# Kernel tuning notes

Measured on AMD Instinct MI355X. Metric: run time of the kernel, lower is better.

## Reference

```python
import jax, jax.numpy as jnp
import numpy as np
from jax import lax

NEG = -1.0e9


def setup_inputs() -> dict:
    key = jax.random.key(0)
    ks = jax.random.split(key, 12)
    B, S, d, H = 4, 1024, 1024, 16
    sc = 1.0 / np.sqrt(d)
    inp = {
        "query": jax.random.normal(ks[0], (B, S, d), jnp.float32),
        "key": jax.random.normal(ks[1], (B, S, d), jnp.float32),
        "value": jax.random.normal(ks[2], (B, S, d), jnp.float32),
        # causal mask: True = masked (future positions)
        "mask": jnp.triu(jnp.ones((S, S), bool), k=1)[None, None],
        "Wq": jax.random.normal(ks[3], (d, d), jnp.float32) * sc,
        "bq": jnp.zeros((d,), jnp.float32),
        "Wk": jax.random.normal(ks[4], (d, d), jnp.float32) * sc,
        "bk": jnp.zeros((d,), jnp.float32),
        "Wv": jax.random.normal(ks[5], (d, d), jnp.float32) * sc,
        "bv": jnp.zeros((d,), jnp.float32),
        "Wo": jax.random.normal(ks[6], (d, d), jnp.float32) * sc,
        "bo": jnp.zeros((d,), jnp.float32),
        "gammas": jax.random.uniform(ks[7], (H, 1, 1), jnp.float32, -0.05, 0.05),
    }
    return inp


def reference(query, key, value, mask, Wq, bq, Wk, bk, Wv, bv, Wo, bo, gammas):
    B, S, d = query.shape
    H = gammas.shape[0]
    dk = d // H

    def proj(x, W, b):
        # [B,S,d] -> [B,H,S,dk]
        return (x @ W.T + b).reshape(B, S, H, dk).transpose(0, 2, 1, 3)

    q = proj(query, Wq, bq)
    k = proj(key, Wk, bk)
    v = proj(value, Wv, bv)

    scores = jnp.einsum("bhqd,bhkd->bhqk", q, k) / np.float32(np.sqrt(dk))

    # --- distance-decay effect (no-grad block in torch) ---
    p = jax.nn.softmax(jnp.where(mask, NEG, scores), axis=-1)
    distcum = jnp.cumsum(p, axis=-1)
    disttot = jnp.sum(p, axis=-1, keepdims=True)
    idx = jnp.arange(S, dtype=scores.dtype)
    pos = jnp.abs(idx[:, None] - idx[None, :])[None, None]  # [1,1,S,S]
    dist = jnp.sqrt(jnp.clip((disttot - distcum) * pos, 0.0))
    dist = lax.stop_gradient(dist)

    gamma = -jnp.abs(gammas)[None]  # [1,H,1,1]
    total_effect = jnp.clip(jnp.exp(dist * gamma), 1e-5, 1e5)

    gated = jnp.where(mask, NEG, scores * total_effect)
    attn = jax.nn.softmax(gated, axis=-1)
    attn = jnp.where(mask, 0.0, attn)

    out = jnp.einsum("bhqk,bhkd->bhqd", attn, v)
    out = out.transpose(0, 2, 1, 3).reshape(B, S, d)
    out = out @ Wo.T + bo
    return out, attn
```

## Files before the change

kernel.cpp:

```cpp
#include <hip/hip_runtime.h>
#include <hip/hip_bf16.h>

typedef __attribute__((ext_vector_type(8))) short short8;
typedef __attribute__((ext_vector_type(4))) float f32x4;
typedef __attribute__((ext_vector_type(4))) unsigned short us4;

#define MFMA(a, b, c) __builtin_amdgcn_mfma_f32_16x16x32_bf16((a), (b), (c), 0, 0, 0)

static __device__ inline unsigned short f2b(float f) {
    __hip_bfloat16 h = __float2bfloat16(f);
    return *reinterpret_cast<unsigned short*>(&h);
}
static __device__ inline float b2f(unsigned short u) {
    unsigned int x = ((unsigned int)u) << 16;
    return __builtin_bit_cast(float, x);
}

static __device__ __forceinline__ void gload_lds16(const unsigned short* g, unsigned short* s) {
    __builtin_amdgcn_global_load_lds(
        (const __attribute__((address_space(1))) unsigned int*)(g),
        (__attribute__((address_space(3))) unsigned int*)(s),
        16, 0, 0);
}

__global__ __launch_bounds__(256) void convk(
    const float* __restrict__ a, const float* __restrict__ b,
    const float* __restrict__ c, const float* __restrict__ dd,
    unsigned short* oa, unsigned short* ob, unsigned short* oc, unsigned short* od, int n)
{
    const float* in; unsigned short* out;
    switch (blockIdx.y) {
        case 0: in = a; out = oa; break;
        case 1: in = b; out = ob; break;
        case 2: in = c; out = oc; break;
        default: in = dd; out = od; break;
    }
    int i = (blockIdx.x * 256 + threadIdx.x) * 4;
    if (i >= n) return;
    float4 v = *(const float4*)(in + i);
    us4 o;
    o[0] = f2b(v.x); o[1] = f2b(v.y); o[2] = f2b(v.z); o[3] = f2b(v.w);
    *(us4*)(out + i) = o;
}

template<int EMODE>
__global__ __launch_bounds__(256) void gemm_bt(
    const unsigned short* __restrict__ A,
    const unsigned short* __restrict__ Bm,
    const float* __restrict__ bias,
    float* __restrict__ Cf,
    unsigned short* __restrict__ Cb,
    int M, int N, int K)
{
    __shared__ unsigned short sA[2][64 * 32];
    __shared__ unsigned short sB[2][128 * 32];
    const int tid = threadIdx.x;
    const int wave = tid >> 6, lane = tid & 63;
    const int wm = (wave >> 1) * 32, wn = (wave & 1) * 64;
    const int bm = blockIdx.x * 64, bn = blockIdx.y * 128;
    const int fr = lane & 15, fg = lane >> 4;

    const int srow = lane >> 2, schk = (lane & 3) * 8;
    const unsigned short* Ab  = A  + (size_t)(bm + wave * 16 + srow) * K + schk;
    const unsigned short* Bb0 = Bm + (size_t)(bn + wave * 32 + srow) * K + schk;
    const unsigned short* Bb1 = Bb0 + (size_t)16 * K;
    const int aw = (wave * 16) * 32, bw0 = (wave * 32) * 32, bw1 = (wave * 32 + 16) * 32;

    f32x4 acc[2][4] = {};
    const int nt = K >> 5;

    gload_lds16(Ab, &sA[0][aw]);
    gload_lds16(Bb0, &sB[0][bw0]);
    gload_lds16(Bb1, &sB[0][bw1]);
    __syncthreads();

    int cur = 0;
    for (int t = 0; t < nt; ++t) {
        if (t + 1 < nt) {
            int kt = (t + 1) << 5;
            gload_lds16(Ab + kt, &sA[cur ^ 1][aw]);
            gload_lds16(Bb0 + kt, &sB[cur ^ 1][bw0]);
            gload_lds16(Bb1 + kt, &sB[cur ^ 1][bw1]);
        }
        short8 af[2], bf[4];
        #pragma unroll
        for (int mr = 0; mr < 2; ++mr) af[mr] = *(const short8*)&sA[cur][(wm + mr * 16 + fr) * 32 + fg * 8];
        #pragma unroll
        for (int nr = 0; nr < 4; ++nr) bf[nr] = *(const short8*)&sB[cur][(wn + nr * 16 + fr) * 32 + fg * 8];
        #pragma unroll
        for (int mr = 0; mr < 2; ++mr)
            #pragma unroll
            for (int nr = 0; nr < 4; ++nr)
                acc[mr][nr] = MFMA(af[mr], bf[nr], acc[mr][nr]);
        __syncthreads();
        cur ^= 1;
    }

    #pragma unroll
    for (int mr = 0; mr < 2; ++mr)
        #pragma unroll
        for (int nr = 0; nr < 4; ++nr)
            #pragma unroll
            for (int j = 0; j < 4; ++j) {
                int m = bm + wm + mr * 16 + fg * 4 + j;
                int n = bn + wn + nr * 16 + fr;
                float v = acc[mr][nr][j] + bias[n];
                if (EMODE == 0) {
                    Cf[(size_t)m * N + n] = v;
                } else if (EMODE == 1) {
                    int b = m >> 10, s = m & 1023, h = n >> 6, dc = n & 63;
                    Cb[(((size_t)(b * 16 + h)) * 1024 + s) * 64 + dc] = f2b(v);
                } else {
                    int b = m >> 10, s = m & 1023, h = n >> 6, dc = n & 63;
                    Cb[(((size_t)(b * 16 + h)) * 64 + dc) * 1024 + s] = f2b(v);
                }
            }
}

__global__ __launch_bounds__(256) void attn_fused(
    const unsigned short* __restrict__ Qh,
    const unsigned short* __restrict__ Kh,
    const unsigned short* __restrict__ Vt,
    const float* __restrict__ gammas,
    float* __restrict__ attn_out,
    unsigned short* __restrict__ ctx)
{
    extern __shared__ char smem[];
    const int RS = 1032;
    unsigned short* s_s = (unsigned short*)smem;
    unsigned short* s_q = (unsigned short*)(smem + 16 * RS * 2);
    float* s_inv = (float*)(smem + 16 * RS * 2 + 16 * 72 * 2);
    const int S = 1024;

    int gid = blockIdx.y * gridDim.x + blockIdx.x;
    int jj = gid >> 3;
    const int bh = (gid & 7) * 8 + (jj >> 6);
    const int qb = jj & 63;
    const int q0 = qb * 16;
    const int tid = threadIdx.x;
    const int wave = tid >> 6, lane = tid & 63, fr = lane & 15, fg = lane >> 4;

    {
        int rr = tid >> 4, c4 = (tid & 15) * 4;
        *(uint2*)&s_q[rr * 72 + c4] = *(const uint2*)&Qh[((size_t)bh * S + q0 + rr) * 64 + c4];
    }
    __syncthreads();
    const int kmax = q0 + 15;

    {
        short8 qf0 = *(const short8*)&s_q[fr * 72 + fg * 8];
        short8 qf1 = *(const short8*)&s_q[fr * 72 + 32 + fg * 8];
        const unsigned short* kbase = &Kh[(size_t)bh * S * 64];
        for (int nf = 0; nf < 16; ++nf) {
            int cb = (nf * 4 + wave) * 16;
            if (cb > kmax) break;
            const unsigned short* kb = kbase + (size_t)cb * 64;
            short8 kf0 = *(const short8*)&kb[fr * 64 + fg * 8];
            short8 kf1 = *(const short8*)&kb[fr * 64 + 32 + fg * 8];
            f32x4 a = {0.f, 0.f, 0.f, 0.f};
            a = MFMA(qf0, kf0, a);
            a = MFMA(qf1, kf1, a);
            #pragma unroll
            for (int j = 0; j < 4; ++j)
                s_s[(size_t)(fg * 4 + j) * RS + cb + fr] = f2b(a[j] * 0.125f);
        }
    }
    __syncthreads();

    {
        const int r = tid >> 4, sub = tid & 15;
        const int qr = q0 + r;
        unsigned short* srow = &s_s[(size_t)r * RS];
        const float ag = fabsf(gammas[bh & 15]);
        const int m = ((qb + 4) >> 2) | 1;
        const int L = 4 * m;
        const int base = sub * L;

        float seg = 0.f;
        for (int c = 0; c < m; ++c) {
            us4 s4 = *(const us4*)&srow[base + c * 4];
            #pragma unroll
            for (int j = 0; j < 4; ++j) {
                int kk = base + c * 4 + j;
                seg += (kk <= qr) ? __expf(b2f(s4[j])) : 0.f;
            }
        }
        float x = seg, t;
        t = __shfl_up(x, 1, 16); if (sub >= 1) x += t;
        t = __shfl_up(x, 2, 16); if (sub >= 2) x += t;
        t = __shfl_up(x, 4, 16); if (sub >= 4) x += t;
        t = __shfl_up(x, 8, 16); if (sub >= 8) x += t;
        const float T = __shfl(x, 15, 16);
        const float invT = 1.f / T;
        float run = x - seg;

        float ls2 = 0.f;
        for (int c = 0; c < m; ++c) {
            us4 s4 = *(const us4*)&srow[base + c * 4];
            us4 o;
            #pragma unroll
            for (int j = 0; j < 4; ++j) {
                int kk = base + c * 4 + j;
                bool act = kk <= qr;
                float s = b2f(s4[j]);
                float e = act ? __expf(s) : 0.f;
                run += e;
                float rem = fmaxf(T - run, 0.f) * invT;
                float dist = sqrtf(rem * (float)(qr - kk));
                float te = __expf(-ag * dist);
                float e2 = act ? __expf(s * te) : 0.f;
                o[j] = f2b(e2);
                ls2 += e2;
            }
            *(us4*)&srow[base + c * 4] = o;
        }
        us4 z = {0, 0, 0, 0};
        for (int c = 4 * L + sub; c < 256; c += 16)
            *(us4*)&srow[c * 4] = z;
        #pragma unroll
        for (int mm = 1; mm < 16; mm <<= 1) ls2 += __shfl_xor(ls2, mm, 16);
        if (sub == 0) s_inv[r] = 1.f / ls2;
    }
    __syncthreads();

    for (int r2 = 0; r2 < 16; ++r2) {
        us4 e4 = *(const us4*)&s_s[(size_t)r2 * RS + tid * 4];
        float iv = s_inv[r2];
        f32x4 w = {b2f(e4[0]) * iv, b2f(e4[1]) * iv, b2f(e4[2]) * iv, b2f(e4[3]) * iv};
        __builtin_nontemporal_store(w,
            (f32x4*)(attn_out + ((size_t)bh * S + q0 + r2) * S + tid * 4));
    }

    {
        const unsigned short* vb = &Vt[(size_t)bh * 64 * S];
        f32x4 acc = {0.f, 0.f, 0.f, 0.f};
        const int ktiles = (kmax + 32) >> 5;
        const unsigned short* prow = &s_s[(size_t)fr * RS];
        for (int kt = 0; kt < ktiles; ++kt) {
            short8 pa = *(const short8*)&prow[kt * 32 + fg * 8];
            short8 vf = *(const short8*)&vb[(size_t)(wave * 16 + fr) * S + kt * 32 + fg * 8];
            acc = MFMA(pa, vf, acc);
        }
        int b = bh >> 4, h = bh & 15;
        #pragma unroll
        for (int j = 0; j < 4; ++j) {
            float iv = s_inv[fg * 4 + j];
            ctx[((size_t)b * S + q0 + fg * 4 + j) * 1024 + h * 64 + wave * 16 + fr] = f2b(acc[j] * iv);
        }
    }
}

extern "C" void kernel_launch(void* const* d_in, const int* in_sizes, int n_in,
                              void* d_out, int out_size, void* d_ws, size_t ws_size,
                              hipStream_t stream) {
    const float* query  = (const float*)d_in[0];
    const float* key    = (const float*)d_in[1];
    const float* value  = (const float*)d_in[2];
    const float* Wq = (const float*)d_in[4];
    const float* bq = (const float*)d_in[5];
    const float* Wk = (const float*)d_in[6];
    const float* bk = (const float*)d_in[7];
    const float* Wv = (const float*)d_in[8];
    const float* bv = (const float*)d_in[9];
    const float* Wo = (const float*)d_in[10];
    const float* bo = (const float*)d_in[11];
    const float* gammas = (const float*)d_in[12];

    const int S = 1024, dmodel = 1024;
    const int M = 4 * S;
    const size_t MD = (size_t)M * dmodel;
    const size_t DD = (size_t)dmodel * dmodel;

    char* ws = (char*)d_ws;
    unsigned short* xq  = (unsigned short*)ws;            ws += MD * 2;
    unsigned short* xk  = (unsigned short*)ws;            ws += MD * 2;
    unsigned short* xv  = (unsigned short*)ws;            ws += MD * 2;
    unsigned short* wqb = (unsigned short*)ws;            ws += DD * 2;
    unsigned short* wkb = (unsigned short*)ws;            ws += DD * 2;
    unsigned short* wvb = (unsigned short*)ws;            ws += DD * 2;
    unsigned short* wob = (unsigned short*)ws;            ws += DD * 2;
    unsigned short* qh  = (unsigned short*)ws;            ws += MD * 2;
    unsigned short* kh  = (unsigned short*)ws;            ws += MD * 2;
    unsigned short* vt  = (unsigned short*)ws;            ws += MD * 2;
    unsigned short* ctx = (unsigned short*)ws;            ws += MD * 2;

    float* outp = (float*)d_out;
    float* attn_out = outp + MD;

    convk<<<dim3(4096, 3), 256, 0, stream>>>(query, key, value, nullptr, xq, xk, xv, nullptr, (int)MD);
    convk<<<dim3(1024, 4), 256, 0, stream>>>(Wq, Wk, Wv, Wo, wqb, wkb, wvb, wob, (int)DD);

    gemm_bt<1><<<dim3(64, 8), 256, 0, stream>>>(xq, wqb, bq, nullptr, qh, M, dmodel, dmodel);
    gemm_bt<1><<<dim3(64, 8), 256, 0, stream>>>(xk, wkb, bk, nullptr, kh, M, dmodel, dmodel);
    gemm_bt<2><<<dim3(64, 8), 256, 0, stream>>>(xv, wvb, bv, nullptr, vt, M, dmodel, dmodel);

    size_t lds = 16 * 1032 * 2 + 16 * 72 * 2 + 16 * 4;
    attn_fused<<<dim3(64, 64), 256, lds, stream>>>(qh, kh, vt, gammas, attn_out, ctx);

    gemm_bt<0><<<dim3(64, 8), 256, 0, stream>>>(ctx, wob, bo, outp, nullptr, M, dmodel, dmodel);
}
```

Measured before the change: 195.0 us.

## Merge conversion and QKV GEMM launches and triple-buffer GEMM loads

Merges the two fp32-to-bf16 conversion launches into one 7-way grid and the three Q/K/V projection GEMMs into one z-indexed launch. This cuts launch overhead and lets more blocks run concurrently. The GEMM main loop moves from double to triple buffering, with a prefetch distance of two tiles, explicit vmcnt waits and raw s_barrier calls in place of __syncthreads. Risks are the extra LDS per block, which may lower occupancy, and whether the hand-written waitcnt counts correctly guard the global-to-LDS loads.

```diff
diff --git a/kernel.cpp b/kernel.cpp
--- a/kernel.cpp
+++ b/kernel.cpp
@@ -24,16 +24,22 @@
 }
 
 __global__ __launch_bounds__(256) void convk(
-    const float* __restrict__ a, const float* __restrict__ b,
-    const float* __restrict__ c, const float* __restrict__ dd,
-    unsigned short* oa, unsigned short* ob, unsigned short* oc, unsigned short* od, int n)
-{
-    const float* in; unsigned short* out;
+    const float* __restrict__ i0, const float* __restrict__ i1, const float* __restrict__ i2,
+    const float* __restrict__ i3, const float* __restrict__ i4, const float* __restrict__ i5,
+    const float* __restrict__ i6,
+    unsigned short* o0, unsigned short* o1, unsigned short* o2, unsigned short* o3,
+    unsigned short* o4, unsigned short* o5, unsigned short* o6,
+    int nbig, int nsmall)
+{
+    const float* in; unsigned short* out; int n;
     switch (blockIdx.y) {
-        case 0: in = a; out = oa; break;
-        case 1: in = b; out = ob; break;
-        case 2: in = c; out = oc; break;
-        default: in = dd; out = od; break;
+        case 0: in = i0; out = o0; n = nbig; break;
+        case 1: in = i1; out = o1; n = nbig; break;
+        case 2: in = i2; out = o2; n = nbig; break;
+        case 3: in = i3; out = o3; n = nsmall; break;
+        case 4: in = i4; out = o4; n = nsmall; break;
+        case 5: in = i5; out = o5; n = nsmall; break;
+        default: in = i6; out = o6; n = nsmall; break;
     }
     int i = (blockIdx.x * 256 + threadIdx.x) * 4;
     if (i >= n) return;
@@ -43,21 +49,19 @@
     *(us4*)(out + i) = o;
 }
 
-template<int EMODE>
-__global__ __launch_bounds__(256) void gemm_bt(
+__device__ __forceinline__ void gemm_body(
     const unsigned short* __restrict__ A,
     const unsigned short* __restrict__ Bm,
     const float* __restrict__ bias,
     float* __restrict__ Cf,
     unsigned short* __restrict__ Cb,
-    int M, int N, int K)
-{
-    __shared__ unsigned short sA[2][64 * 32];
-    __shared__ unsigned short sB[2][128 * 32];
+    int emode, int M, int N, int K, int bmx, int bnx,
+    unsigned short (*sA)[64 * 32], unsigned short (*sB)[128 * 32])
+{
     const int tid = threadIdx.x;
     const int wave = tid >> 6, lane = tid & 63;
     const int wm = (wave >> 1) * 32, wn = (wave & 1) * 64;
-    const int bm = blockIdx.x * 64, bn = blockIdx.y * 128;
+    const int bm = bmx * 64, bn = bnx * 128;
     const int fr = lane & 15, fg = lane >> 4;
 
     const int srow = lane >> 2, schk = (lane & 3) * 8;
@@ -69,19 +73,30 @@
     f32x4 acc[2][4] = {};
     const int nt = K >> 5;
 
-    gload_lds16(Ab, &sA[0][aw]);
-    gload_lds16(Bb0, &sB[0][bw0]);
-    gload_lds16(Bb1, &sB[0][bw1]);
-    __syncthreads();
-
-    int cur = 0;
+    gload_lds16(Ab,       &sA[0][aw]);
+    gload_lds16(Bb0,      &sB[0][bw0]);
+    gload_lds16(Bb1,      &sB[0][bw1]);
+    gload_lds16(Ab + 32,  &sA[1][aw]);
+    gload_lds16(Bb0 + 32, &sB[1][bw0]);
+    gload_lds16(Bb1 + 32, &sB[1][bw1]);
+
     for (int t = 0; t < nt; ++t) {
-        if (t + 1 < nt) {
-            int kt = (t + 1) << 5;
-            gload_lds16(Ab + kt, &sA[cur ^ 1][aw]);
-            gload_lds16(Bb0 + kt, &sB[cur ^ 1][bw0]);
-            gload_lds16(Bb1 + kt, &sB[cur ^ 1][bw1]);
-        }
+        const int cur = t % 3;
+        if (t + 2 < nt) {
+            const int nxt = (t + 2) % 3;
+            const int kt = (t + 2) << 5;
+            gload_lds16(Ab + kt,  &sA[nxt][aw]);
+            gload_lds16(Bb0 + kt, &sB[nxt][bw0]);
+            gload_lds16(Bb1 + kt, &sB[nxt][bw1]);
+            asm volatile("s_waitcnt vmcnt(6)" ::: "memory");
+        } else if (t + 1 < nt) {
+            asm volatile("s_waitcnt vmcnt(3)" ::: "memory");
+        } else {
+            asm volatile("s_waitcnt vmcnt(0)" ::: "memory");
+        }
+        __builtin_amdgcn_s_barrier();
+        __builtin_amdgcn_sched_barrier(0);
+
         short8 af[2], bf[4];
         #pragma unroll
         for (int mr = 0; mr < 2; ++mr) af[mr] = *(const short8*)&sA[cur][(wm + mr * 16 + fr) * 32 + fg * 8];
@@ -92,8 +107,9 @@
             #pragma unroll
             for (int nr = 0; nr < 4; ++nr)
                 acc[mr][nr] = MFMA(af[mr], bf[nr], acc[mr][nr]);
-        __syncthreads();
-        cur ^= 1;
+
+        __builtin_amdgcn_s_barrier();
+        __builtin_amdgcn_sched_barrier(0);
     }
 
     #pragma unroll
@@ -105,9 +121,9 @@
                 int m = bm + wm + mr * 16 + fg * 4 + j;
                 int n = bn + wn + nr * 16 + fr;
                 float v = acc[mr][nr][j] + bias[n];
-                if (EMODE == 0) {
+                if (emode == 0) {
                     Cf[(size_t)m * N + n] = v;
-                } else if (EMODE == 1) {
+                } else if (emode == 1) {
                     int b = m >> 10, s = m & 1023, h = n >> 6, dc = n & 63;
                     Cb[(((size_t)(b * 16 + h)) * 1024 + s) * 64 + dc] = f2b(v);
                 } else {
@@ -115,6 +131,36 @@
                     Cb[(((size_t)(b * 16 + h)) * 64 + dc) * 1024 + s] = f2b(v);
                 }
             }
+}
+
+__global__ __launch_bounds__(256) void gemm_qkv(
+    const unsigned short* __restrict__ xq, const unsigned short* __restrict__ xk,
+    const unsigned short* __restrict__ xv,
+    const unsigned short* __restrict__ wq, const unsigned short* __restrict__ wk,
+    const unsigned short* __restrict__ wv,
+    const float* __restrict__ bq, const float* __restrict__ bk, const float* __restrict__ bv,
+    unsigned short* __restrict__ qh, unsigned short* __restrict__ kh,
+    unsigned short* __restrict__ vt,
+    int M, int N, int K)
+{
+    __shared__ unsigned short sA[3][64 * 32];
+    __shared__ unsigned short sB[3][128 * 32];
+    const int z = blockIdx.z;
+    const unsigned short* A  = z == 0 ? xq : z == 1 ? xk : xv;
+    const unsigned short* Bm = z == 0 ? wq : z == 1 ? wk : wv;
+    const float* bias        = z == 0 ? bq : z == 1 ? bk : bv;
+    unsigned short* Cb       = z == 0 ? qh : z == 1 ? kh : vt;
+    gemm_body(A, Bm, bias, nullptr, Cb, z == 2 ? 2 : 1, M, N, K,
+              blockIdx.x, blockIdx.y, sA, sB);
+}
+
+__global__ __launch_bounds__(256) void gemm_wo(
+    const unsigned short* __restrict__ A, const unsigned short* __restrict__ Bm,
+    const float* __restrict__ bias, float* __restrict__ Cf, int M, int N, int K)
+{
+    __shared__ unsigned short sA[3][64 * 32];
+    __shared__ unsigned short sB[3][128 * 32];
+    gemm_body(A, Bm, bias, Cf, nullptr, 0, M, N, K, blockIdx.x, blockIdx.y, sA, sB);
 }
 
 __global__ __launch_bounds__(256) void attn_fused(
@@ -287,15 +333,15 @@
     float* outp = (float*)d_out;
     float* attn_out = outp + MD;
 
-    convk<<<dim3(4096, 3), 256, 0, stream>>>(query, key, value, nullptr, xq, xk, xv, nullptr, (int)MD);
-    convk<<<dim3(1024, 4), 256, 0, stream>>>(Wq, Wk, Wv, Wo, wqb, wkb, wvb, wob, (int)DD);
-
-    gemm_bt<1><<<dim3(64, 8), 256, 0, stream>>>(xq, wqb, bq, nullptr, qh, M, dmodel, dmodel);
-    gemm_bt<1><<<dim3(64, 8), 256, 0, stream>>>(xk, wkb, bk, nullptr, kh, M, dmodel, dmodel);
-    gemm_bt<2><<<dim3(64, 8), 256, 0, stream>>>(xv, wvb, bv, nullptr, vt, M, dmodel, dmodel);
+    convk<<<dim3(4096, 7), 256, 0, stream>>>(
+        query, key, value, Wq, Wk, Wv, Wo,
+        xq, xk, xv, wqb, wkb, wvb, wob, (int)MD, (int)DD);
+
+    gemm_qkv<<<dim3(64, 8, 3), 256, 0, stream>>>(
+        xq, xk, xv, wqb, wkb, wvb, bq, bk, bv, qh, kh, vt, M, dmodel, dmodel);
 
     size_t lds = 16 * 1032 * 2 + 16 * 72 * 2 + 16 * 4;
     attn_fused<<<dim3(64, 64), 256, lds, stream>>>(qh, kh, vt, gammas, attn_out, ctx);
 
-    gemm_bt<0><<<dim3(64, 8), 256, 0, stream>>>(ctx, wob, bo, outp, nullptr, M, dmodel, dmodel);
-}
+    gemm_wo<<<dim3(64, 8), 256, 0, stream>>>(ctx, wob, bo, outp, M, dmodel, dmodel);
+}
```

Result: faster. 186.1 us (-4.6%).

## Fuse fp32-to-bf16 input conversion into QKV GEMM and triple-buffer GEMM pipelines

Applied to the files above, without the earlier changes.

The separate conversion kernel for query/key/value is removed. The QKV GEMM now loads fp32 activations into registers, converts them to bf16 and writes them to LDS, and all three projections run in one launch over a z-dimension. Both GEMMs now use a K-step of 64 with a 3-stage LDS ring and explicit vmcnt waits and barriers, so loads for tile t+2 overlap compute on tile t. This drops an extra read/write pass over the activations and two kernel launches, at the cost of more LDS per block and hand-tuned waitcnt logic that is fragile.

```diff
diff --git a/kernel.cpp b/kernel.cpp
--- a/kernel.cpp
+++ b/kernel.cpp
@@ -22,18 +22,22 @@
         (__attribute__((address_space(3))) unsigned int*)(s),
         16, 0, 0);
 }
+#define WAITV(N) asm volatile("s_waitcnt vmcnt(" #N ")" ::: "memory")
+#define WAITL    asm volatile("s_waitcnt lgkmcnt(0)" ::: "memory")
+#define SBAR     __builtin_amdgcn_s_barrier()
+#define SCHED0   __builtin_amdgcn_sched_barrier(0)
 
 __global__ __launch_bounds__(256) void convk(
-    const float* __restrict__ a, const float* __restrict__ b,
-    const float* __restrict__ c, const float* __restrict__ dd,
-    unsigned short* oa, unsigned short* ob, unsigned short* oc, unsigned short* od, int n)
+    const float* __restrict__ i0, const float* __restrict__ i1,
+    const float* __restrict__ i2, const float* __restrict__ i3,
+    unsigned short* o0, unsigned short* o1, unsigned short* o2, unsigned short* o3, int n)
 {
     const float* in; unsigned short* out;
     switch (blockIdx.y) {
-        case 0: in = a; out = oa; break;
-        case 1: in = b; out = ob; break;
-        case 2: in = c; out = oc; break;
-        default: in = dd; out = od; break;
+        case 0: in = i0; out = o0; break;
+        case 1: in = i1; out = o1; break;
+        case 2: in = i2; out = o2; break;
+        default: in = i3; out = o3; break;
     }
     int i = (blockIdx.x * 256 + threadIdx.x) * 4;
     if (i >= n) return;
@@ -43,57 +47,98 @@
     *(us4*)(out + i) = o;
 }
 
-template<int EMODE>
-__global__ __launch_bounds__(256) void gemm_bt(
-    const unsigned short* __restrict__ A,
-    const unsigned short* __restrict__ Bm,
-    const float* __restrict__ bias,
-    float* __restrict__ Cf,
-    unsigned short* __restrict__ Cb,
+__global__ __launch_bounds__(256) void gemm_qkv(
+    const float* __restrict__ Aq, const float* __restrict__ Ak, const float* __restrict__ Av,
+    const unsigned short* __restrict__ wq, const unsigned short* __restrict__ wk,
+    const unsigned short* __restrict__ wv,
+    const float* __restrict__ bq, const float* __restrict__ bk, const float* __restrict__ bv,
+    unsigned short* __restrict__ qh, unsigned short* __restrict__ kh,
+    unsigned short* __restrict__ vt,
     int M, int N, int K)
 {
-    __shared__ unsigned short sA[2][64 * 32];
-    __shared__ unsigned short sB[2][128 * 32];
+    __shared__ unsigned short sA[3][2 * 64 * 32];
+    __shared__ unsigned short sB[3][2 * 128 * 32];
+    const int z = blockIdx.z;
+    const float* A           = z == 0 ? Aq : z == 1 ? Ak : Av;
+    const unsigned short* Bm = z == 0 ? wq : z == 1 ? wk : wv;
+    const float* bias        = z == 0 ? bq : z == 1 ? bk : bv;
+    unsigned short* Cb       = z == 0 ? qh : z == 1 ? kh : vt;
+    const int emode          = z == 2 ? 2 : 1;
+
     const int tid = threadIdx.x;
     const int wave = tid >> 6, lane = tid & 63;
     const int wm = (wave >> 1) * 32, wn = (wave & 1) * 64;
     const int bm = blockIdx.x * 64, bn = blockIdx.y * 128;
     const int fr = lane & 15, fg = lane >> 4;
 
-    const int srow = lane >> 2, schk = (lane & 3) * 8;
-    const unsigned short* Ab  = A  + (size_t)(bm + wave * 16 + srow) * K + schk;
-    const unsigned short* Bb0 = Bm + (size_t)(bn + wave * 32 + srow) * K + schk;
-    const unsigned short* Bb1 = Bb0 + (size_t)16 * K;
-    const int aw = (wave * 16) * 32, bw0 = (wave * 32) * 32, bw1 = (wave * 32 + 16) * 32;
+    const int ar = tid >> 2, ac = (tid & 3) * 16;
+    const float* Ag = A + (size_t)(bm + ar) * K + ac;
+    const int aks = ac >> 5, acol = ac & 31;
+    const int brow = lane >> 2, bchk = (lane & 3) * 8;
+    const unsigned short* Bg = Bm + (size_t)(bn + wave * 32 + brow) * K + bchk;
 
     f32x4 acc[2][4] = {};
-    const int nt = K >> 5;
-
-    gload_lds16(Ab, &sA[0][aw]);
-    gload_lds16(Bb0, &sB[0][bw0]);
-    gload_lds16(Bb1, &sB[0][bw1]);
-    __syncthreads();
-
-    int cur = 0;
+    const int nt = K >> 6;
+
+    float4 rA[4];
+    #define LOAD_A(t)  { const float* p = Ag + ((t) << 6); \
+        rA[0] = *(const float4*)(p); rA[1] = *(const float4*)(p + 4); \
+        rA[2] = *(const float4*)(p + 8); rA[3] = *(const float4*)(p + 12); }
+    #define GLOAD_B(buf, t) { const unsigned short* p = Bg + ((t) << 6); \
+        gload_lds16(p,               &sB[buf][(0 * 128 + wave * 32 + 0 ) * 32]); \
+        gload_lds16(p + 16 * K,      &sB[buf][(0 * 128 + wave * 32 + 16) * 32]); \
+        gload_lds16(p + 32,          &sB[buf][(1 * 128 + wave * 32 + 0 ) * 32]); \
+        gload_lds16(p + 16 * K + 32, &sB[buf][(1 * 128 + wave * 32 + 16) * 32]); }
+    #define WRITE_A(buf) { \
+        unsigned short* d = &sA[buf][(aks * 64 + ar) * 32 + acol]; \
+        us4 w0, w1; \
+        w0[0] = f2b(rA[0].x); w0[1] = f2b(rA[0].y); w0[2] = f2b(rA[0].z); w0[3] = f2b(rA[0].w); \
+        w1[0] = f2b(rA[1].x); w1[1] = f2b(rA[1].y); w1[2] = f2b(rA[1].z); w1[3] = f2b(rA[1].w); \
+        *(us4*)(d) = w0; *(us4*)(d + 4) = w1; \
+        w0[0] = f2b(rA[2].x); w0[1] = f2b(rA[2].y); w0[2] = f2b(rA[2].z); w0[3] = f2b(rA[2].w); \
+        w1[0] = f2b(rA[3].x); w1[1] = f2b(rA[3].y); w1[2] = f2b(rA[3].z); w1[3] = f2b(rA[3].w); \
+        *(us4*)(d + 8) = w0; *(us4*)(d + 12) = w1; }
+
+    LOAD_A(0);
+    SCHED0;
+    GLOAD_B(0, 0);
+    WAITV(4);
+    WRITE_A(0);
+    LOAD_A(1);
+    SCHED0;
+    GLOAD_B(1, 1);
+
     for (int t = 0; t < nt; ++t) {
-        if (t + 1 < nt) {
-            int kt = (t + 1) << 5;
-            gload_lds16(Ab + kt, &sA[cur ^ 1][aw]);
-            gload_lds16(Bb0 + kt, &sB[cur ^ 1][bw0]);
-            gload_lds16(Bb1 + kt, &sB[cur ^ 1][bw1]);
-        }
-        short8 af[2], bf[4];
-        #pragma unroll
-        for (int mr = 0; mr < 2; ++mr) af[mr] = *(const short8*)&sA[cur][(wm + mr * 16 + fr) * 32 + fg * 8];
-        #pragma unroll
-        for (int nr = 0; nr < 4; ++nr) bf[nr] = *(const short8*)&sB[cur][(wn + nr * 16 + fr) * 32 + fg * 8];
-        #pragma unroll
-        for (int mr = 0; mr < 2; ++mr)
+        const int cur = t % 3;
+        if (t + 1 < nt) { WAITV(4); } else { WAITV(0); }
+        if (t + 1 < nt) { WRITE_A((t + 1) % 3); }
+        if (t + 2 < nt) {
+            LOAD_A(t + 2);
+            SCHED0;
+            GLOAD_B((t + 2) % 3, t + 2);
+        }
+        WAITL;
+        SBAR; SCHED0;
+
+        short8 af[2][2], bf[4][2];
+        #pragma unroll
+        for (int ks = 0; ks < 2; ++ks) {
+            #pragma unroll
+            for (int mr = 0; mr < 2; ++mr)
+                af[mr][ks] = *(const short8*)&sA[cur][(ks * 64 + wm + mr * 16 + fr) * 32 + fg * 8];
             #pragma unroll
             for (int nr = 0; nr < 4; ++nr)
-                acc[mr][nr] = MFMA(af[mr], bf[nr], acc[mr][nr]);
-        __syncthreads();
-        cur ^= 1;
+                bf[nr][ks] = *(const short8*)&sB[cur][(ks * 128 + wn + nr * 16 + fr) * 32 + fg * 8];
+        }
+        #pragma unroll
+        for (int ks = 0; ks < 2; ++ks)
+            #pragma unroll
+            for (int mr = 0; mr < 2; ++mr)
+                #pragma unroll
+                for (int nr = 0; nr < 4; ++nr)
+                    acc[mr][nr] = MFMA(af[mr][ks], bf[nr][ks], acc[mr][nr]);
+
+        SCHED0; SBAR;
     }
 
     #pragma unroll
@@ -105,15 +150,84 @@
                 int m = bm + wm + mr * 16 + fg * 4 + j;
                 int n = bn + wn + nr * 16 + fr;
                 float v = acc[mr][nr][j] + bias[n];
-                if (EMODE == 0) {
-                    Cf[(size_t)m * N + n] = v;
-                } else if (EMODE == 1) {
-                    int b = m >> 10, s = m & 1023, h = n >> 6, dc = n & 63;
+                int b = m >> 10, s = m & 1023, h = n >> 6, dc = n & 63;
+                if (emode == 1)
                     Cb[(((size_t)(b * 16 + h)) * 1024 + s) * 64 + dc] = f2b(v);
-                } else {
-                    int b = m >> 10, s = m & 1023, h = n >> 6, dc = n & 63;
+                else
                     Cb[(((size_t)(b * 16 + h)) * 64 + dc) * 1024 + s] = f2b(v);
-                }
+            }
+    #undef LOAD_A
+    #undef GLOAD_B
+    #undef WRITE_A
+}
+
+__global__ __launch_bounds__(256) void gemm_wo(
+    const unsigned short* __restrict__ A, const unsigned short* __restrict__ Bm,
+    const float* __restrict__ bias, float* __restrict__ Cf, int M, int N, int K)
+{
+    __shared__ unsigned short sA[3][2 * 64 * 32];
+    __shared__ unsigned short sB[3][2 * 128 * 32];
+    const int tid = threadIdx.x;
+    const int wave = tid >> 6, lane = tid & 63;
+    const int wm = (wave >> 1) * 32, wn = (wave & 1) * 64;
+    const int bm = blockIdx.x * 64, bn = blockIdx.y * 128;
+    const int fr = lane & 15, fg = lane >> 4;
+
+    const int srow = lane >> 2, schk = (lane & 3) * 8;
+    const unsigned short* Ag = A + (size_t)(bm + wave * 16 + srow) * K + schk;
+    const unsigned short* Bg = Bm + (size_t)(bn + wave * 32 + srow) * K + schk;
+
+    #define STAGE(buf, t) { const unsigned short* ap = Ag + ((t) << 6); \
+        gload_lds16(ap,      &sA[buf][(0 * 64 + wave * 16) * 32]); \
+        gload_lds16(ap + 32, &sA[buf][(1 * 64 + wave * 16) * 32]); \
+        const unsigned short* bp = Bg + ((t) << 6); \
+        gload_lds16(bp,               &sB[buf][(0 * 128 + wave * 32 + 0 ) * 32]); \
+        gload_lds16(bp + 16 * K,      &sB[buf][(0 * 128 + wave * 32 + 16) * 32]); \
+        gload_lds16(bp + 32,          &sB[buf][(1 * 128 + wave * 32 + 0 ) * 32]); \
+        gload_lds16(bp + 16 * K + 32, &sB[buf][(1 * 128 + wave * 32 + 16) * 32]); }
+
+    f32x4 acc[2][4] = {};
+    const int nt = K >> 6;
+
+    STAGE(0, 0); STAGE(1, 1);
+    for (int t = 0; t < nt; ++t) {
+        const int cur = t % 3;
+        if (t + 2 < nt)      { STAGE((t + 2) % 3, t + 2); WAITV(12); }
+        else if (t + 1 < nt) { WAITV(6); }
+        else                 { WAITV(0); }
+        SBAR; SCHED0;
+
+        short8 af[2][2], bf[4][2];
+        #pragma unroll
+        for (int ks = 0; ks < 2; ++ks) {
+            #pragma unroll
+            for (int mr = 0; mr < 2; ++mr)
+                af[mr][ks] = *(const short8*)&sA[cur][(ks * 64 + wm + mr * 16 + fr) * 32 + fg * 8];
+            #pragma unroll
+            for (int nr = 0; nr < 4; ++nr)
+                bf[nr][ks] = *(const short8*)&sB[cur][(ks * 128 + wn + nr * 16 + fr) * 32 + fg * 8];
+        }
+        #pragma unroll
+        for (int ks = 0; ks < 2; ++ks)
+            #pragma unroll
+            for (int mr = 0; mr < 2; ++mr)
+                #pragma unroll
+                for (int nr = 0; nr < 4; ++nr)
+                    acc[mr][nr] = MFMA(af[mr][ks], bf[nr][ks], acc[mr][nr]);
+
+        SCHED0; SBAR;
+    }
+    #undef STAGE
+
+    #pragma unroll
+    for (int mr = 0; mr < 2; ++mr)
+        #pragma unroll
+        for (int nr = 0; nr < 4; ++nr)
+            #pragma unroll
+            for (int j = 0; j < 4; ++j) {
+                int m = bm + wm + mr * 16 + fg * 4 + j;
+                int n = bn + wn + nr * 16 + fr;
+                Cf[(size_t)m * N + n] = acc[mr][nr][j] + bias[n];
             }
 }
 
@@ -272,9 +386,6 @@
     const size_t DD = (size_t)dmodel * dmodel;
 
     char* ws = (char*)d_ws;
-    unsigned short* xq  = (unsigned short*)ws;            ws += MD * 2;
-    unsigned short* xk  = (unsigned short*)ws;            ws += MD * 2;
-    unsigned short* xv  = (unsigned short*)ws;            ws += MD * 2;
     unsigned short* wqb = (unsigned short*)ws;            ws += DD * 2;
     unsigned short* wkb = (unsigned short*)ws;            ws += DD * 2;
     unsigned short* wvb = (unsigned short*)ws;            ws += DD * 2;
@@ -287,15 +398,13 @@
     float* outp = (float*)d_out;
     float* attn_out = outp + MD;
 
-    convk<<<dim3(4096, 3), 256, 0, stream>>>(query, key, value, nullptr, xq, xk, xv, nullptr, (int)MD);
     convk<<<dim3(1024, 4), 256, 0, stream>>>(Wq, Wk, Wv, Wo, wqb, wkb, wvb, wob, (int)DD);
 
-    gemm_bt<1><<<dim3(64, 8), 256, 0, stream>>>(xq, wqb, bq, nullptr, qh, M, dmodel, dmodel);
-    gemm_bt<1><<<dim3(64, 8), 256, 0, stream>>>(xk, wkb, bk, nullptr, kh, M, dmodel, dmodel);
-    gemm_bt<2><<<dim3(64, 8), 256, 0, stream>>>(xv, wvb, bv, nullptr, vt, M, dmodel, dmodel);
+    gemm_qkv<<<dim3(64, 8, 3), 256, 0, stream>>>(
+        query, key, value, wqb, wkb, wvb, bq, bk, bv, qh, kh, vt, M, dmodel, dmodel);
 
     size_t lds = 16 * 1032 * 2 + 16 * 72 * 2 + 16 * 4;
     attn_fused<<<dim3(64, 64), 256, lds, stream>>>(qh, kh, vt, gammas, attn_out, ctx);
 
-    gemm_bt<0><<<dim3(64, 8), 256, 0, stream>>>(ctx, wob, bo, outp, nullptr, M, dmodel, dmodel);
-}
+    gemm_wo<<<dim3(64, 8), 256, 0, stream>>>(ctx, wob, bo, outp, M, dmodel, dmodel);
+}
```

Result: faster. 183.9 us (-5.7%).
